# Optimization experiments

Measured on AMD Instinct MI355X. Metric: run time of the kernel, lower is better.

The kernel has to match this reference:

```python
import jax, jax.numpy as jnp
import numpy as np

B, S, R = 8192, 256, 8192  # gas cells, species, reactions


def setup_inputs() -> dict:
    key = jax.random.key(0)
    ks = jax.random.split(key, 10)
    abundances = jax.random.uniform(ks[0], (B, S), jnp.float32, 1e-12, 1.0)
    temperature = jax.random.uniform(ks[1], (B,), jnp.float32, 10.0, 300.0)
    cr_rate = jax.random.uniform(ks[2], (B,), jnp.float32, 0.1, 10.0)
    fuv_rate = jax.random.uniform(ks[3], (B,), jnp.float32, 0.1, 10.0)
    time = jnp.zeros((B,), jnp.float32)  # unused by the RHS, kept for signature parity
    incidence = jax.random.normal(ks[4], (S, R), jnp.float32)  # stoichiometry matrix
    alpha = jax.random.uniform(ks[5], (R,), jnp.float32, 1e-12, 1e-9)
    beta = jax.random.normal(ks[6], (R,), jnp.float32) * 0.5
    gamma = jax.random.uniform(ks[7], (R,), jnp.float32, 0.0, 100.0)
    # species index or S (== out-of-bounds sentinel -> fill_value 1.0, i.e. <2 reactants)
    reactant_multipliers = jax.random.randint(ks[8], (R, 2), 0, S + 1, jnp.int32)
    rtype = jax.random.randint(ks[9], (R,), 0, 3, jnp.int32)  # 0: Arrhenius, 1: CR, 2: FUV
    return {
        'time': time, 'abundances': abundances, 'temperature': temperature,
        'cr_rate': cr_rate, 'fuv_rate': fuv_rate, 'incidence': incidence,
        'alpha': alpha, 'beta': beta, 'gamma': gamma,
        'reactant_multipliers': reactant_multipliers, 'rtype': rtype,
    }


def _get_rates(temperature, cr_rate, fuv_rate, alpha, beta, gamma, rtype):
    # JNetwork.get_rates: hstack of per-reaction rate terms -> (B, R)
    T = temperature[:, None]                                      # (B, 1)
    k_arr = alpha * jnp.exp(beta * jnp.log(T / 300.0) - gamma / T)  # Arrhenius
    k_cr = alpha * cr_rate[:, None]                               # cosmic-ray driven
    k_fuv = alpha * jnp.exp(-gamma) * fuv_rate[:, None]           # FUV photorate
    return jnp.where(rtype == 0, k_arr, jnp.where(rtype == 1, k_cr, k_fuv))


def reference(time, abundances, temperature, cr_rate, fuv_rate,
              incidence, alpha, beta, gamma, reactant_multipliers, rtype):
    rates = _get_rates(temperature, cr_rate, fuv_rate, alpha, beta, gamma, rtype)
    # multiply_rates_by_abundance: gather reactant abundances (mode='drop',
    # fill_value=1.0) and reduce with a product over the 2 reactant slots.
    ones_col = jnp.ones((abundances.shape[0], 1), abundances.dtype)
    ab_pad = jnp.concatenate([abundances, ones_col], axis=1)      # (B, S+1), col S == 1.0
    prod = ab_pad[:, reactant_multipliers[:, 0]] * ab_pad[:, reactant_multipliers[:, 1]]  # (B, R)
    flux = rates * prod                                           # (B, R)
    # incidence @ rates, batched: (S, R) x (B, R) -> (B, S)
    return jnp.einsum('sr,br->bs', incidence, flux)
```

## Files before the change

### kernel.cpp

```cpp
#include <hip/hip_runtime.h>
#include <stdint.h>

typedef __bf16 bf16;
typedef __bf16 bf16x8 __attribute__((ext_vector_type(8)));
typedef float  f32x4  __attribute__((ext_vector_type(4)));

#if __has_builtin(__builtin_amdgcn_exp2f)
#define EXP2F(x) __builtin_amdgcn_exp2f(x)
#else
#define EXP2F(x) exp2f(x)
#endif

constexpr int Bn = 8192, Sn = 256, Rn = 8192;
constexpr int BM = 64, BK = 32, KP = 4;
constexpr int KLEN = Rn / KP;
constexpr int NC = KLEN / BK;

__global__ __launch_bounds__(256) void build_perm(const int* __restrict__ rtype,
                                                  int* __restrict__ perm) {
  __shared__ int c0[256], c1[256], c2[256];
  const int t = threadIdx.x;
  const int base = t * 32;
  int4 vv[8];
  const int4* rp = (const int4*)(rtype + base);
#pragma unroll
  for (int k = 0; k < 8; ++k) vv[k] = rp[k];
  int ty[32];
#pragma unroll
  for (int k = 0; k < 8; ++k) {
    ty[k * 4 + 0] = vv[k].x; ty[k * 4 + 1] = vv[k].y;
    ty[k * 4 + 2] = vv[k].z; ty[k * 4 + 3] = vv[k].w;
  }
  int l0 = 0, l1 = 0, l2 = 0;
#pragma unroll
  for (int i = 0; i < 32; ++i) {
    int v = ty[i];
    l0 += (v == 0); l1 += (v == 1); l2 += (v == 2);
  }
  c0[t] = l0; c1[t] = l1; c2[t] = l2;
  __syncthreads();
  for (int off = 1; off < 256; off <<= 1) {
    int a = (t >= off) ? c0[t - off] : 0;
    int b = (t >= off) ? c1[t - off] : 0;
    int c = (t >= off) ? c2[t - off] : 0;
    __syncthreads();
    c0[t] += a; c1[t] += b; c2[t] += c;
    __syncthreads();
  }
  const int tot0 = c0[255], tot1 = c1[255];
  int o0 = c0[t] - l0;
  int o1 = tot0 + c1[t] - l1;
  int o2 = tot0 + tot1 + c2[t] - l2;
#pragma unroll
  for (int i = 0; i < 32; ++i) {
    int v = ty[i];
    int pos = (v == 0) ? o0++ : ((v == 1) ? o1++ : o2++);
    perm[pos] = base + i;
  }
}

__global__ __launch_bounds__(256) void prep_all(
    const float* __restrict__ inc, bf16* __restrict__ incb,
    const float* __restrict__ alpha, const float* __restrict__ beta,
    const float* __restrict__ gam, const int* __restrict__ rm, const int* __restrict__ rtype,
    float4* __restrict__ params, const float* __restrict__ temp,
    const float* __restrict__ cr, const float* __restrict__ fuv, float4* __restrict__ perb,
    const int* __restrict__ perm) {
  const int g = blockIdx.x, tid = threadIdx.x;
  size_t e = ((size_t)g * 256 + tid) * 8;
  int col8 = (int)(e & 31);
  int row  = (int)((e >> 5) & 255);
  int c    = (int)((e >> 13) & 63);
  int kp   = (int)(e >> 19);
  const int* pp = perm + (kp * KLEN + c * BK + col8);
  const float* rowp = inc + ((size_t)row << 13);
  bf16x8 o;
#pragma unroll
  for (int i = 0; i < 8; ++i) o[i] = (bf16)rowp[pp[i]];
  *(bf16x8*)(incb + e) = o;
  if (g < 32) {
    int p = g * 256 + tid;
    int r = perm[p];
    float a = alpha[r], be = beta[r], gm = gam[r];
    int ty = rtype[r];
    int i0 = rm[2 * r], i1 = rm[2 * r + 1];
    float x, P = 0.0f, Q = 0.0f;
    if (ty == 0) { x = __log2f(a); P = be; Q = gm; }
    else if (ty == 1) { x = a; }
    else { x = a * expf(-gm); }
    uint32_t bits = (uint32_t)i0 | ((uint32_t)i1 << 10) | ((uint32_t)ty << 20);
    params[p] = make_float4(x, P, Q, __uint_as_float(bits));
  } else if (g < 64) {
    int b = (g - 32) * 256 + tid;
    float T = temp[b];
    perb[b] = make_float4(__log2f(T * (1.0f / 300.0f)), 1.4426950408889634f / T,
                          cr[b], fuv[b]);
  }
}

__global__ __launch_bounds__(256, 2) void flux_gemm(
    const float* __restrict__ abund, const float4* __restrict__ perb,
    const float4* __restrict__ params, const bf16* __restrict__ incb,
    float* __restrict__ partial) {
  __shared__ bf16 ab_lds[257 * 64];
  __shared__ bf16 flux_lds[2][64 * BK];

  const int tid  = threadIdx.x;
  const int lane = tid & 63;
  const int w    = tid >> 6;
  const int ws   = __builtin_amdgcn_readfirstlane(w);
  const int x   = blockIdx.x & 7;
  const int jb  = blockIdx.x >> 3;
  const int kp  = x & 3;
  const int m0g = (jb * 2 + (x >> 2)) * BM;
  const int kstart = kp * KLEN;
  const int r16 = lane & 15, q = lane >> 4;
  const int sw16 = (r16 >> 1) & 3;
  const int fsw  = w ^ ((lane >> 1) & 3);

  {
    int bsub = tid >> 2;
    int scol = (tid & 3) * 64;
    const float* rowp = abund + (size_t)(m0g + bsub) * Sn + scol;
#pragma unroll
    for (int j = 0; j < 16; ++j) {
      float4 v = *(const float4*)(rowp + j * 4);
      int s = scol + j * 4;
      ab_lds[(s + 0) * 64 + bsub] = (bf16)v.x;
      ab_lds[(s + 1) * 64 + bsub] = (bf16)v.y;
      ab_lds[(s + 2) * 64 + bsub] = (bf16)v.z;
      ab_lds[(s + 3) * 64 + bsub] = (bf16)v.w;
    }
    if (tid < 64) ab_lds[256 * 64 + tid] = (bf16)1.0f;
  }

  float4 pb = perb[m0g + lane];
  const float l2t = pb.x, nitv = -pb.y, crv = pb.z, fuvv = pb.w;

  auto flux_tile = [&](int kb, int buf) {
    const float4* pw = params + kb + ws * 8;
    float4 pr[8];
#pragma unroll
    for (int j = 0; j < 8; ++j) pr[j] = pw[j];
    uint32_t b0 = __builtin_amdgcn_readfirstlane(__float_as_uint(pr[0].w));
    uint32_t b7 = __builtin_amdgcn_readfirstlane(__float_as_uint(pr[7].w));
    uint32_t t0 = b0 >> 20, t7 = b7 >> 20;
    bf16x8 fv;
    if (t0 == 0 && t7 == 0) {
#pragma unroll
      for (int j = 0; j < 8; ++j) {
        uint32_t bits = __builtin_amdgcn_readfirstlane(__float_as_uint(pr[j].w));
        int i0 = (int)(bits & 1023), i1 = (int)((bits >> 10) & 1023);
        float a0 = (float)ab_lds[i0 * 64 + lane];
        float a1 = (float)ab_lds[i1 * 64 + lane];
        float v = EXP2F(fmaf(pr[j].y, l2t, fmaf(pr[j].z, nitv, pr[j].x)));
        fv[j] = (bf16)(v * (a0 * a1));
      }
    } else if (t0 == t7) {
      float mv = (t0 == 1) ? crv : fuvv;
#pragma unroll
      for (int j = 0; j < 8; ++j) {
        uint32_t bits = __builtin_amdgcn_readfirstlane(__float_as_uint(pr[j].w));
        int i0 = (int)(bits & 1023), i1 = (int)((bits >> 10) & 1023);
        float a0 = (float)ab_lds[i0 * 64 + lane];
        float a1 = (float)ab_lds[i1 * 64 + lane];
        fv[j] = (bf16)((pr[j].x * mv) * (a0 * a1));
      }
    } else {
#pragma unroll
      for (int j = 0; j < 8; ++j) {
        uint32_t bits = __builtin_amdgcn_readfirstlane(__float_as_uint(pr[j].w));
        int i0 = (int)(bits & 1023), i1 = (int)((bits >> 10) & 1023), ms = (int)(bits >> 20);
        float a0 = (float)ab_lds[i0 * 64 + lane];
        float a1 = (float)ab_lds[i1 * 64 + lane];
        float ve = EXP2F(fmaf(pr[j].y, l2t, fmaf(pr[j].z, nitv, pr[j].x)));
        float vm = pr[j].x * ((ms == 1) ? crv : fuvv);
        float v = (ms == 0) ? ve : vm;
        fv[j] = (bf16)(v * (a0 * a1));
      }
    }
    *(bf16x8*)(flux_lds[buf] + lane * BK + fsw * 8) = fv;
  };

  __syncthreads();

  flux_tile(kstart, 0);

  f32x4 acc[4][4];
#pragma unroll
  for (int i = 0; i < 4; ++i)
#pragma unroll
    for (int j = 0; j < 4; ++j) acc[i][j] = (f32x4)0.0f;

  const bf16* bbase = incb + (size_t)(kp * NC) * 8192 + (w * 64 + r16) * BK + q * 8;

  for (int c = 0; c < NC; ++c) {
    const int cur = c & 1, nxt = cur ^ 1;
    __syncthreads();

    bf16x8 bfr[4];
    const bf16* bp = bbase + (size_t)c * 8192;
#pragma unroll
    for (int nt = 0; nt < 4; ++nt)
      bfr[nt] = *(const bf16x8*)(bp + nt * (16 * BK));

    bf16x8 af[4];
#pragma unroll
    for (int mt = 0; mt < 4; ++mt)
      af[mt] = *(const bf16x8*)(flux_lds[cur] + (mt * 16 + r16) * BK + (q ^ sw16) * 8);

    if (c + 1 < NC) flux_tile(kstart + (c + 1) * BK, nxt);

    __builtin_amdgcn_s_setprio(1);
#pragma unroll
    for (int mt = 0; mt < 4; ++mt)
#pragma unroll
      for (int nt = 0; nt < 4; ++nt)
        acc[mt][nt] = __builtin_amdgcn_mfma_f32_16x16x32_bf16(af[mt], bfr[nt], acc[mt][nt], 0, 0, 0);
    __builtin_amdgcn_s_setprio(0);
  }

  float* pout = partial + (size_t)kp * Bn * Sn;
#pragma unroll
  for (int mt = 0; mt < 4; ++mt)
#pragma unroll
    for (int nt = 0; nt < 4; ++nt) {
      int col = w * 64 + nt * 16 + r16;
      int row = m0g + mt * 16 + q * 4;
#pragma unroll
      for (int rg = 0; rg < 4; ++rg)
        pout[(size_t)(row + rg) * Sn + col] = acc[mt][nt][rg];
    }
}

__global__ __launch_bounds__(256) void reduce_k(const float* __restrict__ partial,
                                               float* __restrict__ out) {
  size_t i = ((size_t)blockIdx.x * 256 + threadIdx.x) * 4;
  constexpr size_t NS = (size_t)Bn * Sn;
  float4 a = *(const float4*)(partial + i);
  float4 b = *(const float4*)(partial + NS + i);
  float4 c = *(const float4*)(partial + 2 * NS + i);
  float4 d = *(const float4*)(partial + 3 * NS + i);
  float4 r;
  r.x = (a.x + b.x) + (c.x + d.x);
  r.y = (a.y + b.y) + (c.y + d.y);
  r.z = (a.z + b.z) + (c.z + d.z);
  r.w = (a.w + b.w) + (c.w + d.w);
  *(float4*)(out + i) = r;
}

extern "C" void kernel_launch(void* const* d_in, const int* in_sizes, int n_in,
                              void* d_out, int out_size, void* d_ws, size_t ws_size,
                              hipStream_t stream) {
  const float* abund = (const float*)d_in[1];
  const float* temp  = (const float*)d_in[2];
  const float* cr    = (const float*)d_in[3];
  const float* fuv   = (const float*)d_in[4];
  const float* inc   = (const float*)d_in[5];
  const float* alpha = (const float*)d_in[6];
  const float* beta  = (const float*)d_in[7];
  const float* gam   = (const float*)d_in[8];
  const int*   rm    = (const int*)d_in[9];
  const int*   rty   = (const int*)d_in[10];
  float* out = (float*)d_out;

  float4* params  = (float4*)d_ws;
  float4* perb    = params + Rn;
  bf16*   incb    = (bf16*)(perb + Bn);
  float*  partial = (float*)(incb + (size_t)Sn * Rn);
  int*    perm    = (int*)partial;

  build_perm<<<1, 256, 0, stream>>>(rty, perm);
  prep_all<<<1024, 256, 0, stream>>>(inc, incb, alpha, beta, gam, rm, rty,
                                     params, temp, cr, fuv, perb, perm);
  flux_gemm<<<(Bn / BM) * KP, 256, 0, stream>>>(abund, perb, params, incb, partial);
  reduce_k<<<(Bn * Sn) / 1024, 256, 0, stream>>>(partial, out);
}
```

Baseline: 159.5 us.

## Stage incidence rows in LDS for permute and raise split-K to eight

The incidence permute/convert kernel now stages one full incidence row per block in shared memory and gathers from LDS, replacing scattered global gathers. The GEMM is templated on split-K factor and uses 8 K-partitions when workspace allows, doubling grid size for better CU fill, with launch bounds raised to 3 blocks per CU. The reduce kernel sums 8 partials in that case, which doubles partial-buffer write and read traffic.

```diff
diff --git a/kernel.cpp b/kernel.cpp
--- a/kernel.cpp
+++ b/kernel.cpp
@@ -12,9 +12,7 @@
 #endif
 
 constexpr int Bn = 8192, Sn = 256, Rn = 8192;
-constexpr int BM = 64, BK = 32, KP = 4;
-constexpr int KLEN = Rn / KP;
-constexpr int NC = KLEN / BK;
+constexpr int BM = 64, BK = 32;
 
 __global__ __launch_bounds__(256) void build_perm(const int* __restrict__ rtype,
                                                   int* __restrict__ perm) {
@@ -66,20 +64,27 @@
     float4* __restrict__ params, const float* __restrict__ temp,
     const float* __restrict__ cr, const float* __restrict__ fuv, float4* __restrict__ perb,
     const int* __restrict__ perm) {
-  const int g = blockIdx.x, tid = threadIdx.x;
-  size_t e = ((size_t)g * 256 + tid) * 8;
-  int col8 = (int)(e & 31);
-  int row  = (int)((e >> 5) & 255);
-  int c    = (int)((e >> 13) & 63);
-  int kp   = (int)(e >> 19);
-  const int* pp = perm + (kp * KLEN + c * BK + col8);
-  const float* rowp = inc + ((size_t)row << 13);
-  bf16x8 o;
-#pragma unroll
-  for (int i = 0; i < 8; ++i) o[i] = (bf16)rowp[pp[i]];
-  *(bf16x8*)(incb + e) = o;
+  __shared__ __align__(16) float row_lds[8192];
+  const int g = blockIdx.x, t = threadIdx.x;
+  const float* rowp = inc + ((size_t)g << 13);
+#pragma unroll
+  for (int i = 0; i < 8; ++i)
+    *(float4*)(row_lds + (i * 256 + t) * 4) = *(const float4*)(rowp + (i * 256 + t) * 4);
+  __syncthreads();
+  const int4* pq = (const int4*)(perm + t * 32);
+  bf16* outp = incb + ((size_t)t * 256 + g) * 32;
+#pragma unroll
+  for (int k8 = 0; k8 < 4; ++k8) {
+    int4 pa = pq[k8 * 2], pb = pq[k8 * 2 + 1];
+    bf16x8 o;
+    o[0] = (bf16)row_lds[pa.x]; o[1] = (bf16)row_lds[pa.y];
+    o[2] = (bf16)row_lds[pa.z]; o[3] = (bf16)row_lds[pa.w];
+    o[4] = (bf16)row_lds[pb.x]; o[5] = (bf16)row_lds[pb.y];
+    o[6] = (bf16)row_lds[pb.z]; o[7] = (bf16)row_lds[pb.w];
+    *(bf16x8*)(outp + k8 * 8) = o;
+  }
   if (g < 32) {
-    int p = g * 256 + tid;
+    int p = g * 256 + t;
     int r = perm[p];
     float a = alpha[r], be = beta[r], gm = gam[r];
     int ty = rtype[r];
@@ -91,17 +96,20 @@
     uint32_t bits = (uint32_t)i0 | ((uint32_t)i1 << 10) | ((uint32_t)ty << 20);
     params[p] = make_float4(x, P, Q, __uint_as_float(bits));
   } else if (g < 64) {
-    int b = (g - 32) * 256 + tid;
+    int b = (g - 32) * 256 + t;
     float T = temp[b];
     perb[b] = make_float4(__log2f(T * (1.0f / 300.0f)), 1.4426950408889634f / T,
                           cr[b], fuv[b]);
   }
 }
 
-__global__ __launch_bounds__(256, 2) void flux_gemm(
+template <int KP>
+__global__ __launch_bounds__(256, 3) void flux_gemm(
     const float* __restrict__ abund, const float4* __restrict__ perb,
     const float4* __restrict__ params, const bf16* __restrict__ incb,
     float* __restrict__ partial) {
+  constexpr int KLEN = Rn / KP;
+  constexpr int NC   = KLEN / BK;
   __shared__ bf16 ab_lds[257 * 64];
   __shared__ bf16 flux_lds[2][64 * BK];
 
@@ -109,10 +117,11 @@
   const int lane = tid & 63;
   const int w    = tid >> 6;
   const int ws   = __builtin_amdgcn_readfirstlane(w);
-  const int x   = blockIdx.x & 7;
-  const int jb  = blockIdx.x >> 3;
-  const int kp  = x & 3;
-  const int m0g = (jb * 2 + (x >> 2)) * BM;
+  const int x  = blockIdx.x & 7;
+  const int jb = blockIdx.x >> 3;
+  int kp, m0g;
+  if constexpr (KP == 8) { kp = x;     m0g = jb * BM; }
+  else                   { kp = x & 3; m0g = (jb * 2 + (x >> 2)) * BM; }
   const int kstart = kp * KLEN;
   const int r16 = lane & 15, q = lane >> 4;
   const int sw16 = (r16 >> 1) & 3;
@@ -192,7 +201,7 @@
 #pragma unroll
     for (int j = 0; j < 4; ++j) acc[i][j] = (f32x4)0.0f;
 
-  const bf16* bbase = incb + (size_t)(kp * NC) * 8192 + (w * 64 + r16) * BK + q * 8;
+  const bf16* bbase = incb + (size_t)(kstart / BK) * 8192 + (w * 64 + r16) * BK + q * 8;
 
   for (int c = 0; c < NC; ++c) {
     const int cur = c & 1, nxt = cur ^ 1;
@@ -233,6 +242,7 @@
     }
 }
 
+template <int KP>
 __global__ __launch_bounds__(256) void reduce_k(const float* __restrict__ partial,
                                                float* __restrict__ out) {
   size_t i = ((size_t)blockIdx.x * 256 + threadIdx.x) * 4;
@@ -246,6 +256,16 @@
   r.y = (a.y + b.y) + (c.y + d.y);
   r.z = (a.z + b.z) + (c.z + d.z);
   r.w = (a.w + b.w) + (c.w + d.w);
+  if constexpr (KP == 8) {
+    float4 e = *(const float4*)(partial + 4 * NS + i);
+    float4 f = *(const float4*)(partial + 5 * NS + i);
+    float4 g = *(const float4*)(partial + 6 * NS + i);
+    float4 h = *(const float4*)(partial + 7 * NS + i);
+    r.x += (e.x + f.x) + (g.x + h.x);
+    r.y += (e.y + f.y) + (g.y + h.y);
+    r.z += (e.z + f.z) + (g.z + h.z);
+    r.w += (e.w + f.w) + (g.w + h.w);
+  }
   *(float4*)(out + i) = r;
 }
 
@@ -270,9 +290,18 @@
   float*  partial = (float*)(incb + (size_t)Sn * Rn);
   int*    perm    = (int*)partial;
 
+  const size_t fixed = (size_t)Rn * 16 + (size_t)Bn * 16 + (size_t)Sn * Rn * 2;
+  const size_t need8 = fixed + 8ull * Bn * Sn * 4;
+  const bool kp8 = ws_size >= need8;
+
   build_perm<<<1, 256, 0, stream>>>(rty, perm);
-  prep_all<<<1024, 256, 0, stream>>>(inc, incb, alpha, beta, gam, rm, rty,
-                                     params, temp, cr, fuv, perb, perm);
-  flux_gemm<<<(Bn / BM) * KP, 256, 0, stream>>>(abund, perb, params, incb, partial);
-  reduce_k<<<(Bn * Sn) / 1024, 256, 0, stream>>>(partial, out);
-}
+  prep_all<<<256, 256, 0, stream>>>(inc, incb, alpha, beta, gam, rm, rty,
+                                    params, temp, cr, fuv, perb, perm);
+  if (kp8) {
+    flux_gemm<8><<<(Bn / BM) * 8, 256, 0, stream>>>(abund, perb, params, incb, partial);
+    reduce_k<8><<<(Bn * Sn) / 1024, 256, 0, stream>>>(partial, out);
+  } else {
+    flux_gemm<4><<<(Bn / BM) * 4, 256, 0, stream>>>(abund, perb, params, incb, partial);
+    reduce_k<4><<<(Bn * Sn) / 1024, 256, 0, stream>>>(partial, out);
+  }
+}
```

Result: slower. 168.0 us (+5.3%).

## Fuse permutation build into prep and fold K-split reduction into GEMM

Applied to the files above, without the earlier changes.

Each prep block now recomputes the rtype-sorted permutation in LDS instead of running a separate single-block kernel. The incidence matrix is permuted and converted to bf16 through an LDS row staging buffer, so global reads are coalesced rather than scattered gathers. The separate reduce kernel is removed: the last of the four K-split blocks for each output tile, detected with an atomic counter, sums the partials and writes the output. This cuts two launches and the scattered reads, at the cost of redundant prefix-sum work per block, a serialized tail reduction, and per-tile counters that must be reset every call.

```diff
diff --git a/kernel.cpp b/kernel.cpp
--- a/kernel.cpp
+++ b/kernel.cpp
@@ -16,25 +16,33 @@
 constexpr int KLEN = Rn / KP;
 constexpr int NC = KLEN / BK;
 
-__global__ __launch_bounds__(256) void build_perm(const int* __restrict__ rtype,
-                                                  int* __restrict__ perm) {
+__global__ __launch_bounds__(256) void prep_all(
+    const float* __restrict__ inc, bf16* __restrict__ incb,
+    const float* __restrict__ alpha, const float* __restrict__ beta,
+    const float* __restrict__ gam, const int* __restrict__ rm, const int* __restrict__ rtype,
+    float4* __restrict__ params, const float* __restrict__ temp,
+    const float* __restrict__ cr, const float* __restrict__ fuv, float4* __restrict__ perb,
+    int* __restrict__ counters) {
+  __shared__ __align__(16) float row_lds[8192];
+  __shared__ unsigned short perm_lds[8192];
   __shared__ int c0[256], c1[256], c2[256];
-  const int t = threadIdx.x;
-  const int base = t * 32;
-  int4 vv[8];
-  const int4* rp = (const int4*)(rtype + base);
-#pragma unroll
-  for (int k = 0; k < 8; ++k) vv[k] = rp[k];
+  const int g = blockIdx.x, t = threadIdx.x;
+
+  int* rt = (int*)row_lds;
+  {
+    const int4* src = (const int4*)rtype;
+    int4* dst = (int4*)rt;
+#pragma unroll
+    for (int i = 0; i < 8; ++i) dst[i * 256 + t] = src[i * 256 + t];
+  }
+  __syncthreads();
+
   int ty[32];
-#pragma unroll
-  for (int k = 0; k < 8; ++k) {
-    ty[k * 4 + 0] = vv[k].x; ty[k * 4 + 1] = vv[k].y;
-    ty[k * 4 + 2] = vv[k].z; ty[k * 4 + 3] = vv[k].w;
-  }
   int l0 = 0, l1 = 0, l2 = 0;
 #pragma unroll
   for (int i = 0; i < 32; ++i) {
-    int v = ty[i];
+    int v = rt[i * 256 + t];
+    ty[i] = v;
     l0 += (v == 0); l1 += (v == 1); l2 += (v == 2);
   }
   c0[t] = l0; c1[t] = l1; c2[t] = l2;
@@ -55,55 +63,58 @@
   for (int i = 0; i < 32; ++i) {
     int v = ty[i];
     int pos = (v == 0) ? o0++ : ((v == 1) ? o1++ : o2++);
-    perm[pos] = base + i;
-  }
-}
-
-__global__ __launch_bounds__(256) void prep_all(
-    const float* __restrict__ inc, bf16* __restrict__ incb,
-    const float* __restrict__ alpha, const float* __restrict__ beta,
-    const float* __restrict__ gam, const int* __restrict__ rm, const int* __restrict__ rtype,
-    float4* __restrict__ params, const float* __restrict__ temp,
-    const float* __restrict__ cr, const float* __restrict__ fuv, float4* __restrict__ perb,
-    const int* __restrict__ perm) {
-  const int g = blockIdx.x, tid = threadIdx.x;
-  size_t e = ((size_t)g * 256 + tid) * 8;
-  int col8 = (int)(e & 31);
-  int row  = (int)((e >> 5) & 255);
-  int c    = (int)((e >> 13) & 63);
-  int kp   = (int)(e >> 19);
-  const int* pp = perm + (kp * KLEN + c * BK + col8);
-  const float* rowp = inc + ((size_t)row << 13);
-  bf16x8 o;
-#pragma unroll
-  for (int i = 0; i < 8; ++i) o[i] = (bf16)rowp[pp[i]];
-  *(bf16x8*)(incb + e) = o;
+    perm_lds[pos] = (unsigned short)(i * 256 + t);
+  }
+  __syncthreads();
+
   if (g < 32) {
-    int p = g * 256 + tid;
-    int r = perm[p];
+    int p = g * 256 + t;
+    int r = perm_lds[p];
     float a = alpha[r], be = beta[r], gm = gam[r];
-    int ty = rtype[r];
+    int tv = rt[r];
     int i0 = rm[2 * r], i1 = rm[2 * r + 1];
     float x, P = 0.0f, Q = 0.0f;
-    if (ty == 0) { x = __log2f(a); P = be; Q = gm; }
-    else if (ty == 1) { x = a; }
+    if (tv == 0) { x = __log2f(a); P = be; Q = gm; }
+    else if (tv == 1) { x = a; }
     else { x = a * expf(-gm); }
-    uint32_t bits = (uint32_t)i0 | ((uint32_t)i1 << 10) | ((uint32_t)ty << 20);
+    uint32_t bits = (uint32_t)i0 | ((uint32_t)i1 << 10) | ((uint32_t)tv << 20);
     params[p] = make_float4(x, P, Q, __uint_as_float(bits));
   } else if (g < 64) {
-    int b = (g - 32) * 256 + tid;
+    int b = (g - 32) * 256 + t;
     float T = temp[b];
     perb[b] = make_float4(__log2f(T * (1.0f / 300.0f)), 1.4426950408889634f / T,
                           cr[b], fuv[b]);
+  } else if (g == 64 && t < 128) {
+    counters[t] = 0;
+  }
+  __syncthreads();
+
+  {
+    const float4* src = (const float4*)(inc + ((size_t)g << 13));
+    float4* dst = (float4*)row_lds;
+#pragma unroll
+    for (int i = 0; i < 8; ++i) dst[i * 256 + t] = src[i * 256 + t];
+  }
+  __syncthreads();
+
+  const unsigned short* pp = perm_lds + t * 32;
+  bf16* outp = incb + ((size_t)t * 256 + g) * 32;
+#pragma unroll
+  for (int k8 = 0; k8 < 4; ++k8) {
+    bf16x8 o;
+#pragma unroll
+    for (int i = 0; i < 8; ++i) o[i] = (bf16)row_lds[pp[k8 * 8 + i]];
+    *(bf16x8*)(outp + k8 * 8) = o;
   }
 }
 
 __global__ __launch_bounds__(256, 2) void flux_gemm(
     const float* __restrict__ abund, const float4* __restrict__ perb,
     const float4* __restrict__ params, const bf16* __restrict__ incb,
-    float* __restrict__ partial) {
+    float* __restrict__ partial, float* __restrict__ out, int* __restrict__ counters) {
   __shared__ bf16 ab_lds[257 * 64];
   __shared__ bf16 flux_lds[2][64 * BK];
+  __shared__ int is_last;
 
   const int tid  = threadIdx.x;
   const int lane = tid & 63;
@@ -192,7 +203,7 @@
 #pragma unroll
     for (int j = 0; j < 4; ++j) acc[i][j] = (f32x4)0.0f;
 
-  const bf16* bbase = incb + (size_t)(kp * NC) * 8192 + (w * 64 + r16) * BK + q * 8;
+  const bf16* bbase = incb + (size_t)(kstart / BK) * 8192 + (w * 64 + r16) * BK + q * 8;
 
   for (int c = 0; c < NC; ++c) {
     const int cur = c & 1, nxt = cur ^ 1;
@@ -231,22 +242,33 @@
       for (int rg = 0; rg < 4; ++rg)
         pout[(size_t)(row + rg) * Sn + col] = acc[mt][nt][rg];
     }
-}
-
-__global__ __launch_bounds__(256) void reduce_k(const float* __restrict__ partial,
-                                               float* __restrict__ out) {
-  size_t i = ((size_t)blockIdx.x * 256 + threadIdx.x) * 4;
-  constexpr size_t NS = (size_t)Bn * Sn;
-  float4 a = *(const float4*)(partial + i);
-  float4 b = *(const float4*)(partial + NS + i);
-  float4 c = *(const float4*)(partial + 2 * NS + i);
-  float4 d = *(const float4*)(partial + 3 * NS + i);
-  float4 r;
-  r.x = (a.x + b.x) + (c.x + d.x);
-  r.y = (a.y + b.y) + (c.y + d.y);
-  r.z = (a.z + b.z) + (c.z + d.z);
-  r.w = (a.w + b.w) + (c.w + d.w);
-  *(float4*)(out + i) = r;
+
+  __threadfence();
+  __syncthreads();
+  const int tile = jb * 2 + (x >> 2);
+  if (tid == 0) is_last = (atomicAdd(&counters[tile], 1) == KP - 1);
+  __syncthreads();
+  if (is_last) {
+    __threadfence();
+    const float4* p4 = (const float4*)partial;
+    float4* o4 = (float4*)out;
+    constexpr size_t NS4 = (size_t)Bn * Sn / 4;
+    const size_t base = (size_t)m0g * (Sn / 4);
+#pragma unroll
+    for (int ii = 0; ii < 16; ++ii) {
+      size_t f = base + (size_t)ii * 256 + tid;
+      float4 a = p4[f];
+      float4 b = p4[NS4 + f];
+      float4 c = p4[2 * NS4 + f];
+      float4 d = p4[3 * NS4 + f];
+      float4 r;
+      r.x = (a.x + b.x) + (c.x + d.x);
+      r.y = (a.y + b.y) + (c.y + d.y);
+      r.z = (a.z + b.z) + (c.z + d.z);
+      r.w = (a.w + b.w) + (c.w + d.w);
+      o4[f] = r;
+    }
+  }
 }
 
 extern "C" void kernel_launch(void* const* d_in, const int* in_sizes, int n_in,
@@ -268,11 +290,10 @@
   float4* perb    = params + Rn;
   bf16*   incb    = (bf16*)(perb + Bn);
   float*  partial = (float*)(incb + (size_t)Sn * Rn);
-  int*    perm    = (int*)partial;
-
-  build_perm<<<1, 256, 0, stream>>>(rty, perm);
-  prep_all<<<1024, 256, 0, stream>>>(inc, incb, alpha, beta, gam, rm, rty,
-                                     params, temp, cr, fuv, perb, perm);
-  flux_gemm<<<(Bn / BM) * KP, 256, 0, stream>>>(abund, perb, params, incb, partial);
-  reduce_k<<<(Bn * Sn) / 1024, 256, 0, stream>>>(partial, out);
+  int*    counters = (int*)(partial + (size_t)KP * Bn * Sn);
+
+  prep_all<<<256, 256, 0, stream>>>(inc, incb, alpha, beta, gam, rm, rty,
+                                    params, temp, cr, fuv, perb, counters);
+  flux_gemm<<<(Bn / BM) * KP, 256, 0, stream>>>(abund, perb, params, incb,
+                                                partial, out, counters);
 }
```

After: 288.7 us. +81.0%, slower.
